# Performance work log

Measured on AMD Instinct MI355X. Metric: run time of the kernel, lower is better.

Reference implementation:

```python
import jax, jax.numpy as jnp
import numpy as np

N_NODES = 100000
N_EDGES = 1000000
F_IN = 256
HID = 256
HID2 = 128
N_CLS = 2


def setup_inputs() -> dict:
    key = jax.random.key(0)
    ks = jax.random.split(key, 8)
    x = jax.random.normal(ks[0], (N_NODES, F_IN), dtype=jnp.float32)
    edge_index = jax.random.randint(ks[1], (2, N_EDGES), 0, N_NODES, dtype=jnp.int64)
    s = lambda k, shp: jax.random.normal(k, shp, dtype=jnp.float32) / np.sqrt(shp[0])
    return {
        "x": x,
        "edge_index": edge_index,
        "W1l": s(ks[2], (F_IN, HID)),
        "W1r": s(ks[3], (F_IN, HID)),
        "b1": jnp.zeros((HID,), jnp.float32),
        "W2l": s(ks[4], (HID, HID2)),
        "W2r": s(ks[5], (HID, HID2)),
        "b2": jnp.zeros((HID2,), jnp.float32),
        "Wc": s(ks[6], (HID2, N_CLS)),
        "bc": jnp.zeros((N_CLS,), jnp.float32),
    }


def _sage_conv(x, src, dst, deg_inv, Wl, Wr, b):
    # mean-aggregate neighbor (source) features at each destination node
    msg = x[src]                                              # [E, F]
    agg = jax.ops.segment_sum(msg, dst, num_segments=N_NODES)  # [N, F]
    mean = agg * deg_inv[:, None]                             # zero for isolated nodes
    return mean @ Wl + b + x @ Wr


def reference(x, edge_index, W1l, W1r, b1, W2l, W2r, b2, Wc, bc):
    src, dst = edge_index[0], edge_index[1]
    cnt = jax.ops.segment_sum(jnp.ones((N_EDGES,), x.dtype), dst, num_segments=N_NODES)
    deg_inv = jnp.where(cnt > 0, 1.0 / jnp.maximum(cnt, 1.0), 0.0)
    h = jax.nn.relu(_sage_conv(x, src, dst, deg_inv, W1l, W1r, b1))   # dropout is identity in eval
    h = jax.nn.relu(_sage_conv(h, src, dst, deg_inv, W2l, W2r, b2))
    logits = h @ Wc + bc
    return jax.nn.log_softmax(logits, axis=1)
```

## Files before the change

kernel.cpp:

```cpp
#include <hip/hip_runtime.h>
#include <hip/hip_bf16.h>

#define NN 100000
#define NE 1000000
#define MPAD 100096
#define MT64  1564
#define MTP64 1568
#define NG1   (MTP64 * 8)
#define NFB   (NE / 64)
#define NDB   ((NE + 255) / 256)
#define NCB   (MPAD / 8)

typedef __attribute__((ext_vector_type(8))) short bf16x8;
typedef __attribute__((ext_vector_type(4))) float f32x4;
typedef __attribute__((ext_vector_type(2))) float f32x2;
typedef __attribute__((ext_vector_type(8))) unsigned short us8;

static __device__ __forceinline__ float bf2f(unsigned short u){
  unsigned int x = ((unsigned int)u) << 16;
  return __uint_as_float(x);
}
static __device__ __forceinline__ unsigned short f2bf(float f){
  unsigned int x = __float_as_uint(f);
  unsigned int r = (x + 0x7fffu + ((x >> 16) & 1u)) >> 16;
  return (unsigned short)r;
}
static __device__ __forceinline__ void addv(float* acc, us8 v){
  #pragma unroll
  for (int k = 0; k < 8; k++) acc[k] += bf2f(v[k]);
}
static __device__ __forceinline__ unsigned char f2fp8(float f){
  unsigned int u = __float_as_uint(f);
  unsigned int s = (u >> 24) & 0x80u;
  float av = fabsf(f);
  if (av >= 448.f) return (unsigned char)(s | 0x7Eu);
  if (av < 0.015625f){
    int m = (int)(av * 512.0f + 0.5f);
    return (unsigned char)(s | (unsigned)m);
  }
  unsigned int au = u & 0x7FFFFFFFu;
  unsigned int r = au + 0x7FFFFu + ((au >> 20) & 1u);
  return (unsigned char)(s | ((r >> 20) - 960u));
}
#if !__has_builtin(__builtin_amdgcn_cvt_pk_f32_fp8)
static __device__ __forceinline__ float fp8tof(unsigned char b){
  unsigned int s = ((unsigned int)(b & 0x80u)) << 24;
  unsigned int e = (b >> 3) & 0xFu, m = b & 7u;
  float v = (e == 0) ? ((float)m * 0.001953125f)
                     : __uint_as_float(((e + 120u) << 23) | (m << 20));
  return __uint_as_float(__float_as_uint(v) | s);
}
#endif
static __device__ __forceinline__ void addq(float* acc, uint2 v){
#if __has_builtin(__builtin_amdgcn_cvt_pk_f32_fp8)
  f32x2 p0 = __builtin_amdgcn_cvt_pk_f32_fp8((int)v.x, false);
  f32x2 p1 = __builtin_amdgcn_cvt_pk_f32_fp8((int)v.x, true);
  f32x2 p2 = __builtin_amdgcn_cvt_pk_f32_fp8((int)v.y, false);
  f32x2 p3 = __builtin_amdgcn_cvt_pk_f32_fp8((int)v.y, true);
  acc[0] += p0[0]; acc[1] += p0[1]; acc[2] += p1[0]; acc[3] += p1[1];
  acc[4] += p2[0]; acc[5] += p2[1]; acc[6] += p3[0]; acc[7] += p3[1];
#else
  unsigned int a = v.x, b = v.y;
  acc[0] += fp8tof(a & 0xFF);         acc[1] += fp8tof((a >> 8) & 0xFF);
  acc[2] += fp8tof((a >> 16) & 0xFF); acc[3] += fp8tof(a >> 24);
  acc[4] += fp8tof(b & 0xFF);         acc[5] += fp8tof((b >> 8) & 0xFF);
  acc[6] += fp8tof((b >> 16) & 0xFF); acc[7] += fp8tof(b >> 24);
#endif
}
static __device__ __forceinline__ void gld16(const void* g, void* l){
  __builtin_amdgcn_global_load_lds((const __attribute__((address_space(1))) void*)g,
                                   (__attribute__((address_space(3))) void*)l, 16, 0, 0);
}


__global__ __launch_bounds__(256)
void k_dc(const int* __restrict__ dst, int* __restrict__ cnt,
          const float* __restrict__ x, unsigned short* __restrict__ xb,
          const float* __restrict__ W1l, const float* __restrict__ W1r,
          const float* __restrict__ W2l, const float* __restrict__ W2r,
          unsigned short* __restrict__ Bt1, unsigned short* __restrict__ Bt2)
{
  const int bid = blockIdx.x, t = threadIdx.x;
  int role, idx;
  if (bid < 2 * NDB){
    role = bid & 1;
    idx = bid >> 1;
  } else if (bid < NDB + NCB){
    role = 0; idx = bid - NDB;
  } else {
    role = 2; idx = bid - NDB - NCB;
  }

  if (role == 1){
    int e = idx * 256 + t;
    if (e < NE) atomicAdd(&cnt[dst[e]], 1);
  } else if (role == 0){
    size_t i = ((size_t)idx * 256 + t) * 8;
    if (i >= (size_t)MPAD * 256) return;
    int row = (int)(i >> 8);
    us8 o;
    if (row < NN){
      const float4* p = (const float4*)(x + i);
      float4 a = p[0], b = p[1];
      o[0]=f2bf(a.x); o[1]=f2bf(a.y); o[2]=f2bf(a.z); o[3]=f2bf(a.w);
      o[4]=f2bf(b.x); o[5]=f2bf(b.y); o[6]=f2bf(b.z); o[7]=f2bf(b.w);
    } else {
      #pragma unroll
      for (int j = 0; j < 8; j++) o[j] = 0;
    }
    *(us8*)(xb + i) = o;
  } else {
    int i = idx * 256 + t;
    if (i < 512 * 256){
      int n = i >> 8, k = i & 255;
      float v = (n < 256) ? W1l[k * 256 + n] : W1r[k * 256 + (n - 256)];
      Bt1[n * 256 + k] = f2bf(v);
    }
    if (i < 256 * 256){
      int n = i >> 8, k = i & 255;
      float v = (n < 128) ? W2l[k * 128 + n] : W2r[k * 128 + (n - 128)];
      Bt2[n * 256 + k] = f2bf(v);
    }
  }
}


__global__ void k_chunk_sum(const int* __restrict__ cnt, int* __restrict__ partials, int N){
  __shared__ int sw[16];
  int b = blockIdx.x, t = threadIdx.x;
  int i = b * 1024 + t;
  int v = (i < N) ? cnt[i] : 0;
  #pragma unroll
  for (int off = 32; off; off >>= 1) v += __shfl_xor(v, off);
  int lane = t & 63, w = t >> 6;
  if (lane == 0) sw[w] = v;
  __syncthreads();
  if (t < 16){
    int s = sw[t];
    #pragma unroll
    for (int off = 8; off; off >>= 1) s += __shfl_xor(s, off);
    if (t == 0) partials[b] = s;
  }
}

__global__ void k_chunk_scan(const int* __restrict__ cnt, const int* __restrict__ partials,
                             int nchunk,
                             int* __restrict__ offs, int* __restrict__ cursor,
                             float* __restrict__ deginv, int N){
  __shared__ int sd[1024];
  __shared__ int sp[128];
  int b = blockIdx.x, t = threadIdx.x;
  if (t < 128) sp[t] = (t < b && t < nchunk) ? partials[t] : 0;
  int i = b * 1024 + t;
  int v = (i < N) ? cnt[i] : 0;
  sd[t] = v;
  __syncthreads();
  #pragma unroll
  for (int off = 64; off; off >>= 1){
    if (t < off) sp[t] += sp[t + off];
    __syncthreads();
  }
  for (int off = 1; off < 1024; off <<= 1){
    int x = (t >= off) ? sd[t - off] : 0;
    __syncthreads();
    sd[t] += x;
    __syncthreads();
  }
  if (i < N){
    int excl = sp[0] + sd[t] - v;
    offs[i] = excl;
    cursor[i] = excl;
    deginv[i] = (v > 0) ? (1.0f / (float)v) : 0.0f;
  }
}


static __device__ __forceinline__
void gemm_tile_db(const unsigned short* __restrict__ A,
                  const unsigned short* __restrict__ Bt,
                  unsigned short* lA, unsigned short* lB,
                  int lane, int m0, int n0,
                  f32x4 (*acc)[4])
{
  const int srow = lane >> 3;
  const int sc   = (lane & 7) ^ ((lane >> 3) & 7);
  #pragma unroll
  for (int s = 0; s < 8; ++s){
    int row = s * 8 + srow;
    gld16(A  + (size_t)(m0 + row) * 256 + sc * 8, &lA[s * 512]);
    gld16(Bt + (size_t)(n0 + row) * 256 + sc * 8, &lB[s * 512]);
  }
  #pragma unroll
  for (int kt = 0; kt < 4; ++kt){
    const int cur = (kt & 1) * 4096;
    if (kt < 3){
      const int nxt = ((kt + 1) & 1) * 4096;
      asm volatile("s_waitcnt lgkmcnt(0)" ::: "memory");
      #pragma unroll
      for (int s = 0; s < 8; ++s){
        int row = s * 8 + srow;
        gld16(A  + (size_t)(m0 + row) * 256 + (kt + 1) * 64 + sc * 8, &lA[nxt + s * 512]);
        gld16(Bt + (size_t)(n0 + row) * 256 + (kt + 1) * 64 + sc * 8, &lB[nxt + s * 512]);
      }
      asm volatile("s_waitcnt vmcnt(16)" ::: "memory");
    } else {
      asm volatile("s_waitcnt vmcnt(0)" ::: "memory");
    }
    __builtin_amdgcn_sched_barrier(0);
    #pragma unroll
    for (int ks = 0; ks < 2; ++ks){
      bf16x8 av[4], bv[4];
      const int kc = ks * 4 + (lane >> 4);
      #pragma unroll
      for (int m = 0; m < 4; m++){
        int r = m * 16 + (lane & 15);
        av[m] = *(const bf16x8*)&lA[cur + r * 64 + ((kc ^ (r & 7)) << 3)];
      }
      #pragma unroll
      for (int n = 0; n < 4; n++){
        int c = n * 16 + (lane & 15);
        bv[n] = *(const bf16x8*)&lB[cur + c * 64 + ((kc ^ (c & 7)) << 3)];
      }
      #pragma unroll
      for (int m = 0; m < 4; m++)
        #pragma unroll
        for (int n = 0; n < 4; n++)
          acc[m][n] = __builtin_amdgcn_mfma_f32_16x16x32_bf16(av[m], bv[n], acc[m][n], 0, 0, 0);
    }
  }
}


__global__ __launch_bounds__(64)
void k_fg(const unsigned short* __restrict__ A,
          const unsigned short* __restrict__ Bt,
          unsigned short* __restrict__ R1,
          unsigned char* __restrict__ Q8,
          const int* __restrict__ src, const int* __restrict__ dst,
          int* __restrict__ cursor, int* __restrict__ csr)
{
  __shared__ __align__(16) unsigned short lA[2 * 64 * 64];
  __shared__ __align__(16) unsigned short lB[2 * 64 * 64];
  const int bid = blockIdx.x;
  const int lane = threadIdx.x & 63;

  bool isg; int idx;
  if (bid < 2 * NG1){
    isg = (bid & 15) < 8;
    idx = ((bid >> 4) << 3) + (bid & 7);
  } else {
    isg = false; idx = bid - NG1;
  }

  if (!isg){
    int e = idx * 64 + lane;
    if (e < NE){
      int p = atomicAdd(&cursor[dst[e]], 1);
      csr[p] = src[e];
    }
    return;
  }

  const int xcd = idx & 7, j = idx >> 3;
  const int mt  = xcd * (MTP64 / 8) + (j >> 3);
  if (mt >= MT64) return;
  const int nt  = j & 7;
  const int m0  = mt * 64;
  const int n0  = nt * 64;

  f32x4 acc[4][4] = {};
  gemm_tile_db(A, Bt, lA, lB, lane, m0, n0, acc);

  const int crow0 = m0 + (lane >> 4) * 4;
  const int ccol0 = n0 + (lane & 15);
  if (n0 < 256){
    #pragma unroll
    for (int m = 0; m < 4; m++){
      #pragma unroll
      for (int r = 0; r < 4; r++){
        size_t rowoff = (size_t)(crow0 + m * 16 + r) * 256;
        #pragma unroll
        for (int n = 0; n < 4; n++)
          Q8[rowoff + ccol0 + n * 16] = f2fp8(acc[m][n][r]);
      }
    }
  } else {
    const int cbase = ccol0 - 256;
    #pragma unroll
    for (int m = 0; m < 4; m++){
      #pragma unroll
      for (int r = 0; r < 4; r++){
        size_t rowoff = (size_t)(crow0 + m * 16 + r) * 256;
        #pragma unroll
        for (int n = 0; n < 4; n++)
          R1[rowoff + cbase + n * 16] = f2bf(acc[m][n][r]);
      }
    }
  }
}


template<int NTL2>
__global__ __launch_bounds__(64)
void k_gemm(const unsigned short* __restrict__ A,
            const unsigned short* __restrict__ Bt,
            unsigned short* __restrict__ C)
{
  const int bid = blockIdx.x;
  const int xcd = bid & 7, j = bid >> 3;
  const int mt  = xcd * (MTP64 / 8) + (j >> NTL2);
  if (mt >= MT64) return;
  const int nt  = j & ((1 << NTL2) - 1);
  const int m0  = mt * 64;
  const int n0  = nt * 64;
  const int Nout = 64 << NTL2;

  __shared__ __align__(16) unsigned short lA[2 * 64 * 64];
  __shared__ __align__(16) unsigned short lB[2 * 64 * 64];
  const int lane = threadIdx.x & 63;

  f32x4 acc[4][4] = {};
  gemm_tile_db(A, Bt, lA, lB, lane, m0, n0, acc);

  const int crow0 = m0 + (lane >> 4) * 4;
  const int ccol0 = n0 + (lane & 15);
  #pragma unroll
  for (int m = 0; m < 4; m++){
    #pragma unroll
    for (int r = 0; r < 4; r++){
      size_t rowoff = (size_t)(crow0 + m * 16 + r) * Nout;
      #pragma unroll
      for (int n = 0; n < 4; n++)
        C[rowoff + ccol0 + n * 16] = f2bf(acc[m][n][r]);
    }
  }
}


__global__ void k_agg1(const unsigned char* __restrict__ Q8,
                       const unsigned short* __restrict__ R1,
                       const float* __restrict__ b1,
                       const int* __restrict__ offs, const int* __restrict__ cnt,
                       const float* __restrict__ deginv,
                       const int* __restrict__ csr,
                       unsigned short* __restrict__ h, int N)
{
  int wv = threadIdx.x >> 6, lane = threadIdx.x & 63;
  int n = blockIdx.x * 4 + wv;
  if (n >= N) return;
  int beg = offs[n], d = cnt[n];
  const int g = lane >> 5;
  const int cl = lane & 31;
  const unsigned char* Qb = Q8 + cl * 8;

  float acc[8];
  #pragma unroll
  for (int k = 0; k < 8; k++) acc[k] = 0.f;

  for (int w0 = 0; w0 < d; w0 += 64){
    int wlen = min(d - w0, 64);
    int idx = 0;
    if (lane < wlen) idx = csr[beg + w0 + lane];
    int nIter = (wlen + 15) >> 4;
    for (int t = 0; t < nIter; t++){
      int e0 = t * 16 + g;
      int s0 = __shfl(idx, e0);
      int s1 = __shfl(idx, e0 + 2);
      int s2 = __shfl(idx, e0 + 4);
      int s3 = __shfl(idx, e0 + 6);
      int s4 = __shfl(idx, e0 + 8);
      int s5 = __shfl(idx, e0 + 10);
      int s6 = __shfl(idx, e0 + 12);
      int s7 = __shfl(idx, e0 + 14);
      uint2 v0 = *(const uint2*)(Qb + (size_t)s0 * 256);
      uint2 v1 = *(const uint2*)(Qb + (size_t)s1 * 256);
      uint2 v2 = *(const uint2*)(Qb + (size_t)s2 * 256);
      uint2 v3 = *(const uint2*)(Qb + (size_t)s3 * 256);
      uint2 v4 = *(const uint2*)(Qb + (size_t)s4 * 256);
      uint2 v5 = *(const uint2*)(Qb + (size_t)s5 * 256);
      uint2 v6 = *(const uint2*)(Qb + (size_t)s6 * 256);
      uint2 v7 = *(const uint2*)(Qb + (size_t)s7 * 256);
      if (e0 < wlen)      addq(acc, v0);
      if (e0 + 2 < wlen)  addq(acc, v1);
      if (e0 + 4 < wlen)  addq(acc, v2);
      if (e0 + 6 < wlen)  addq(acc, v3);
      if (e0 + 8 < wlen)  addq(acc, v4);
      if (e0 + 10 < wlen) addq(acc, v5);
      if (e0 + 12 < wlen) addq(acc, v6);
      if (e0 + 14 < wlen) addq(acc, v7);
    }
  }
  #pragma unroll
  for (int k = 0; k < 8; k++) acc[k] += __shfl_xor(acc[k], 32);

  if (lane < 32){
    float di = deginv[n];
    us8 rv = *(const us8*)(R1 + (size_t)n * 256 + cl * 8);
    float4 b0 = *(const float4*)(b1 + cl * 8);
    float4 b4 = *(const float4*)(b1 + cl * 8 + 4);
    float bb[8] = {b0.x, b0.y, b0.z, b0.w, b4.x, b4.y, b4.z, b4.w};
    us8 o;
    #pragma unroll
    for (int k = 0; k < 8; k++)
      o[k] = f2bf(fmaxf(acc[k] * di + bf2f(rv[k]) + bb[k], 0.f));
    *(us8*)(h + (size_t)n * 256 + cl * 8) = o;
  }
}


__global__ void k_agg2cls(const unsigned short* __restrict__ C2,
                          const float* __restrict__ b2,
                          const float* __restrict__ Wc,
                          const float* __restrict__ bc,
                          const int* __restrict__ offs, const int* __restrict__ cnt,
                          const float* __restrict__ deginv,
                          const int* __restrict__ csr,
                          float* __restrict__ out, int N)
{
  int wv = threadIdx.x >> 6, lane = threadIdx.x & 63;
  int n = blockIdx.x * 4 + wv;
  if (n >= N) return;
  int beg = offs[n], d = cnt[n];
  const int g = lane >> 4;
  const int cl = lane & 15;

  float acc[8];
  #pragma unroll
  for (int k = 0; k < 8; k++) acc[k] = 0.f;

  for (int w0 = 0; w0 < d; w0 += 64){
    int wlen = min(d - w0, 64);
    int idx = 0;
    if (lane < wlen) idx = csr[beg + w0 + lane];
    int nIter = (wlen + 31) >> 5;
    for (int t = 0; t < nIter; t++){
      int e0 = t * 32 + g;
      int s0 = __shfl(idx, e0);
      int s1 = __shfl(idx, e0 + 4);
      int s2 = __shfl(idx, e0 + 8);
      int s3 = __shfl(idx, e0 + 12);
      int s4 = __shfl(idx, e0 + 16);
      int s5 = __shfl(idx, e0 + 20);
      int s6 = __shfl(idx, e0 + 24);
      int s7 = __shfl(idx, e0 + 28);
      us8 v0 = *(const us8*)(C2 + (size_t)s0 * 256 + cl * 8);
      us8 v1 = *(const us8*)(C2 + (size_t)s1 * 256 + cl * 8);
      us8 v2 = *(const us8*)(C2 + (size_t)s2 * 256 + cl * 8);
      us8 v3 = *(const us8*)(C2 + (size_t)s3 * 256 + cl * 8);
      us8 v4 = *(const us8*)(C2 + (size_t)s4 * 256 + cl * 8);
      us8 v5 = *(const us8*)(C2 + (size_t)s5 * 256 + cl * 8);
      us8 v6 = *(const us8*)(C2 + (size_t)s6 * 256 + cl * 8);
      us8 v7 = *(const us8*)(C2 + (size_t)s7 * 256 + cl * 8);
      if (e0 < wlen)      addv(acc, v0);
      if (e0 + 4 < wlen)  addv(acc, v1);
      if (e0 + 8 < wlen)  addv(acc, v2);
      if (e0 + 12 < wlen) addv(acc, v3);
      if (e0 + 16 < wlen) addv(acc, v4);
      if (e0 + 20 < wlen) addv(acc, v5);
      if (e0 + 24 < wlen) addv(acc, v6);
      if (e0 + 28 < wlen) addv(acc, v7);
    }
  }
  #pragma unroll
  for (int k = 0; k < 8; k++){
    acc[k] += __shfl_xor(acc[k], 16);
    acc[k] += __shfl_xor(acc[k], 32);
  }

  float di = deginv[n];
  us8 rv = *(const us8*)(C2 + (size_t)n * 256 + 128 + cl * 8);
  float4 b0 = *(const float4*)(b2 + cl * 8);
  float4 b4 = *(const float4*)(b2 + cl * 8 + 4);
  float bb[8] = {b0.x, b0.y, b0.z, b0.w, b4.x, b4.y, b4.z, b4.w};
  float p0 = 0.f, p1 = 0.f;
  #pragma unroll
  for (int k = 0; k < 8; k += 2){
    float h0 = fmaxf(acc[k]     * di + bf2f(rv[k])     + bb[k],     0.f);
    float h1 = fmaxf(acc[k + 1] * di + bf2f(rv[k + 1]) + bb[k + 1], 0.f);
    float4 w = *(const float4*)(Wc + (cl * 8 + k) * 2);
    p0 += h0 * w.x + h1 * w.z;
    p1 += h0 * w.y + h1 * w.w;
  }
  #pragma unroll
  for (int off = 8; off; off >>= 1){
    p0 += __shfl_xor(p0, off);
    p1 += __shfl_xor(p1, off);
  }
  if (lane == 0){
    float z0 = p0 + bc[0], z1 = p1 + bc[1];
    float m = fmaxf(z0, z1);
    float lse = m + logf(expf(z0 - m) + expf(z1 - m));
    out[(size_t)n * 2 + 0] = z0 - lse;
    out[(size_t)n * 2 + 1] = z1 - lse;
  }
}


extern "C" void kernel_launch(void* const* d_in, const int* in_sizes, int n_in,
                              void* d_out, int out_size, void* d_ws, size_t ws_size,
                              hipStream_t stream)
{
  const float* x   = (const float*)d_in[0];
  const int*   ei  = (const int*)d_in[1];
  const float* W1l = (const float*)d_in[2];
  const float* W1r = (const float*)d_in[3];
  const float* b1  = (const float*)d_in[4];
  const float* W2l = (const float*)d_in[5];
  const float* W2r = (const float*)d_in[6];
  const float* b2  = (const float*)d_in[7];
  const float* Wc  = (const float*)d_in[8];
  const float* bc  = (const float*)d_in[9];
  float* out = (float*)d_out;

  const int N = NN, E = NE;
  const int* src = ei;
  const int* dst = ei + E;

  char* ws = (char*)d_ws;
  size_t off = 0;
  auto alloc = [&](size_t bytes) -> void* {
    void* p = ws + off;
    off += (bytes + 255) & ~(size_t)255;
    return p;
  };
  int*   cnt      = (int*)alloc((size_t)N * 4);
  int*   offs     = (int*)alloc((size_t)N * 4);
  int*   cursor   = (int*)alloc((size_t)N * 4);
  float* deginv   = (float*)alloc((size_t)N * 4);
  int*   partials = (int*)alloc(1024);
  int*   csr      = (int*)alloc((size_t)E * 4);
  unsigned short* Bt1 = (unsigned short*)alloc((size_t)512 * 256 * 2);
  unsigned short* Bt2 = (unsigned short*)alloc((size_t)256 * 256 * 2);
  unsigned short* xb  = (unsigned short*)alloc((size_t)MPAD * 256 * 2);
  unsigned char*  Q8  = (unsigned char*)alloc((size_t)MPAD * 256);
  unsigned short* R1  = (unsigned short*)alloc((size_t)MPAD * 256 * 2);

  unsigned short* h  = xb;
  unsigned short* C2 = R1;

  (void)in_sizes; (void)n_in; (void)out_size; (void)ws_size;

  hipMemsetAsync(cnt, 0, (size_t)N * 4, stream);

  k_dc<<<NDB + NCB + 512, 256, 0, stream>>>(dst, cnt, x, xb, W1l, W1r, W2l, W2r, Bt1, Bt2);

  int nchunk = (N + 1023) / 1024;
  k_chunk_sum<<<nchunk, 1024, 0, stream>>>(cnt, partials, N);
  k_chunk_scan<<<nchunk, 1024, 0, stream>>>(cnt, partials, nchunk, offs, cursor, deginv, N);

  k_fg<<<NG1 + NFB, 64, 0, stream>>>(xb, Bt1, R1, Q8, src, dst, cursor, csr);

  k_agg1<<<N / 4, 256, 0, stream>>>(Q8, R1, b1, offs, cnt, deginv, csr, h, N);

  k_gemm<2><<<MTP64 * 4, 64, 0, stream>>>(h, Bt2, C2);
  k_agg2cls<<<N / 4, 256, 0, stream>>>(C2, b2, Wc, bc, offs, cnt, deginv, csr, out, N);
}
```

Measured before the change: 358.0 us.

## Pack two single-wave GEMM tiles per block and drop LDS double buffering

GEMM blocks now hold two waves, and each wave computes its own independent 64x64 tile with a private single-buffered LDS region. This replaces the software double-buffered K loop with a plain load-wait-compute loop. The edge-to-CSR fill blocks are widened to 128 threads to match. The intent is to halve the block count and rely on two waves per block, plus the freed LDS, for latency hiding instead of in-wave prefetch. The risk is that each wave now stalls on every K-slice load, since nothing inside the wave overlaps loads with compute.

```diff
diff --git a/kernel.cpp b/kernel.cpp
--- a/kernel.cpp
+++ b/kernel.cpp
@@ -7,9 +7,12 @@
 #define MT64  1564
 #define MTP64 1568
 #define NG1   (MTP64 * 8)
-#define NFB   (NE / 64)
+#define NGH   (NG1 / 2)
+#define NFW   ((NE + 127) / 128)
 #define NDB   ((NE + 255) / 256)
 #define NCB   (MPAD / 8)
+#define NT2   (MTP64 * 4)
+#define NT2H  (NT2 / 2)
 
 typedef __attribute__((ext_vector_type(8))) short bf16x8;
 typedef __attribute__((ext_vector_type(4))) float f32x4;
@@ -176,36 +179,23 @@
 
 
 static __device__ __forceinline__
-void gemm_tile_db(const unsigned short* __restrict__ A,
-                  const unsigned short* __restrict__ Bt,
-                  unsigned short* lA, unsigned short* lB,
-                  int lane, int m0, int n0,
-                  f32x4 (*acc)[4])
+void gemm_tile(const unsigned short* __restrict__ A,
+               const unsigned short* __restrict__ Bt,
+               unsigned short* lA, unsigned short* lB,
+               int lane, int m0, int n0,
+               f32x4 (*acc)[4])
 {
   const int srow = lane >> 3;
   const int sc   = (lane & 7) ^ ((lane >> 3) & 7);
-  #pragma unroll
-  for (int s = 0; s < 8; ++s){
-    int row = s * 8 + srow;
-    gld16(A  + (size_t)(m0 + row) * 256 + sc * 8, &lA[s * 512]);
-    gld16(Bt + (size_t)(n0 + row) * 256 + sc * 8, &lB[s * 512]);
-  }
-  #pragma unroll
   for (int kt = 0; kt < 4; ++kt){
-    const int cur = (kt & 1) * 4096;
-    if (kt < 3){
-      const int nxt = ((kt + 1) & 1) * 4096;
-      asm volatile("s_waitcnt lgkmcnt(0)" ::: "memory");
-      #pragma unroll
-      for (int s = 0; s < 8; ++s){
-        int row = s * 8 + srow;
-        gld16(A  + (size_t)(m0 + row) * 256 + (kt + 1) * 64 + sc * 8, &lA[nxt + s * 512]);
-        gld16(Bt + (size_t)(n0 + row) * 256 + (kt + 1) * 64 + sc * 8, &lB[nxt + s * 512]);
-      }
-      asm volatile("s_waitcnt vmcnt(16)" ::: "memory");
-    } else {
-      asm volatile("s_waitcnt vmcnt(0)" ::: "memory");
-    }
+    asm volatile("s_waitcnt lgkmcnt(0)" ::: "memory");
+    #pragma unroll
+    for (int s = 0; s < 8; ++s){
+      int row = s * 8 + srow;
+      gld16(A  + (size_t)(m0 + row) * 256 + kt * 64 + sc * 8, &lA[s * 512]);
+      gld16(Bt + (size_t)(n0 + row) * 256 + kt * 64 + sc * 8, &lB[s * 512]);
+    }
+    asm volatile("s_waitcnt vmcnt(0)" ::: "memory");
     __builtin_amdgcn_sched_barrier(0);
     #pragma unroll
     for (int ks = 0; ks < 2; ++ks){
@@ -214,12 +204,12 @@
       #pragma unroll
       for (int m = 0; m < 4; m++){
         int r = m * 16 + (lane & 15);
-        av[m] = *(const bf16x8*)&lA[cur + r * 64 + ((kc ^ (r & 7)) << 3)];
+        av[m] = *(const bf16x8*)&lA[r * 64 + ((kc ^ (r & 7)) << 3)];
       }
       #pragma unroll
       for (int n = 0; n < 4; n++){
         int c = n * 16 + (lane & 15);
-        bv[n] = *(const bf16x8*)&lB[cur + c * 64 + ((kc ^ (c & 7)) << 3)];
+        bv[n] = *(const bf16x8*)&lB[c * 64 + ((kc ^ (c & 7)) << 3)];
       }
       #pragma unroll
       for (int m = 0; m < 4; m++)
@@ -231,7 +221,7 @@
 }
 
 
-__global__ __launch_bounds__(64)
+__global__ __launch_bounds__(128)
 void k_fg(const unsigned short* __restrict__ A,
           const unsigned short* __restrict__ Bt,
           unsigned short* __restrict__ R1,
@@ -239,21 +229,23 @@
           const int* __restrict__ src, const int* __restrict__ dst,
           int* __restrict__ cursor, int* __restrict__ csr)
 {
-  __shared__ __align__(16) unsigned short lA[2 * 64 * 64];
-  __shared__ __align__(16) unsigned short lB[2 * 64 * 64];
+  __shared__ __align__(16) unsigned short lA[2][64 * 64];
+  __shared__ __align__(16) unsigned short lB[2][64 * 64];
   const int bid = blockIdx.x;
+  const int wv = threadIdx.x >> 6;
   const int lane = threadIdx.x & 63;
 
-  bool isg; int idx;
-  if (bid < 2 * NG1){
+  bool isg; int gi;
+  if (bid < 2 * NGH){
     isg = (bid & 15) < 8;
-    idx = ((bid >> 4) << 3) + (bid & 7);
+    gi = ((bid >> 4) << 3) + (bid & 7);
   } else {
-    isg = false; idx = bid - NG1;
+    isg = false;
+    gi = NGH + (bid - 2 * NGH);
   }
 
   if (!isg){
-    int e = idx * 64 + lane;
+    int e = gi * 128 + wv * 64 + lane;
     if (e < NE){
       int p = atomicAdd(&cursor[dst[e]], 1);
       csr[p] = src[e];
@@ -261,7 +253,8 @@
     return;
   }
 
-  const int xcd = idx & 7, j = idx >> 3;
+  const int t = gi + wv * NGH;
+  const int xcd = t & 7, j = t >> 3;
   const int mt  = xcd * (MTP64 / 8) + (j >> 3);
   if (mt >= MT64) return;
   const int nt  = j & 7;
@@ -269,7 +262,7 @@
   const int n0  = nt * 64;
 
   f32x4 acc[4][4] = {};
-  gemm_tile_db(A, Bt, lA, lB, lane, m0, n0, acc);
+  gemm_tile(A, Bt, &lA[wv][0], &lB[wv][0], lane, m0, n0, acc);
 
   const int crow0 = m0 + (lane >> 4) * 4;
   const int ccol0 = n0 + (lane & 15);
@@ -300,27 +293,27 @@
 }
 
 
-template<int NTL2>
-__global__ __launch_bounds__(64)
-void k_gemm(const unsigned short* __restrict__ A,
-            const unsigned short* __restrict__ Bt,
-            unsigned short* __restrict__ C)
-{
+__global__ __launch_bounds__(128)
+void k_gemm2(const unsigned short* __restrict__ A,
+             const unsigned short* __restrict__ Bt,
+             unsigned short* __restrict__ C)
+{
+  __shared__ __align__(16) unsigned short lA[2][64 * 64];
+  __shared__ __align__(16) unsigned short lB[2][64 * 64];
   const int bid = blockIdx.x;
-  const int xcd = bid & 7, j = bid >> 3;
-  const int mt  = xcd * (MTP64 / 8) + (j >> NTL2);
+  const int wv = threadIdx.x >> 6;
+  const int lane = threadIdx.x & 63;
+
+  const int t = bid + wv * NT2H;
+  const int xcd = t & 7, j = t >> 3;
+  const int mt  = xcd * (MTP64 / 8) + (j >> 2);
   if (mt >= MT64) return;
-  const int nt  = j & ((1 << NTL2) - 1);
+  const int nt  = j & 3;
   const int m0  = mt * 64;
   const int n0  = nt * 64;
-  const int Nout = 64 << NTL2;
-
-  __shared__ __align__(16) unsigned short lA[2 * 64 * 64];
-  __shared__ __align__(16) unsigned short lB[2 * 64 * 64];
-  const int lane = threadIdx.x & 63;
 
   f32x4 acc[4][4] = {};
-  gemm_tile_db(A, Bt, lA, lB, lane, m0, n0, acc);
+  gemm_tile(A, Bt, &lA[wv][0], &lB[wv][0], lane, m0, n0, acc);
 
   const int crow0 = m0 + (lane >> 4) * 4;
   const int ccol0 = n0 + (lane & 15);
@@ -328,7 +321,7 @@
   for (int m = 0; m < 4; m++){
     #pragma unroll
     for (int r = 0; r < 4; r++){
-      size_t rowoff = (size_t)(crow0 + m * 16 + r) * Nout;
+      size_t rowoff = (size_t)(crow0 + m * 16 + r) * 256;
       #pragma unroll
       for (int n = 0; n < 4; n++)
         C[rowoff + ccol0 + n * 16] = f2bf(acc[m][n][r]);
@@ -548,10 +541,13 @@
   k_chunk_sum<<<nchunk, 1024, 0, stream>>>(cnt, partials, N);
   k_chunk_scan<<<nchunk, 1024, 0, stream>>>(cnt, partials, nchunk, offs, cursor, deginv, N);
 
-  k_fg<<<NG1 + NFB, 64, 0, stream>>>(xb, Bt1, R1, Q8, src, dst, cursor, csr);
+  {
+    int nblk = 2 * NGH + (NFW - NGH);
+    k_fg<<<nblk, 128, 0, stream>>>(xb, Bt1, R1, Q8, src, dst, cursor, csr);
+  }
 
   k_agg1<<<N / 4, 256, 0, stream>>>(Q8, R1, b1, offs, cnt, deginv, csr, h, N);
 
-  k_gemm<2><<<MTP64 * 4, 64, 0, stream>>>(h, Bt2, C2);
+  k_gemm2<<<NT2H, 128, 0, stream>>>(h, Bt2, C2);
   k_agg2cls<<<N / 4, 256, 0, stream>>>(C2, b2, Wc, bc, offs, cnt, deginv, csr, out, N);
 }
```

Result: faster. 316.0 us (-11.7%).
